# Performance work log

Hardware: AMD Instinct MI355X
Metric: run time of the kernel (lower is better)

The kernel has to match this reference:

```python
import jax, jax.numpy as jnp
import numpy as np

N, E = 100000, 1600000
IN, H, OUT = 64, 64, 32
BN_EPS = 1e-5


def setup_inputs() -> dict:
    key = jax.random.key(0)
    ks = jax.random.split(key, 13)

    def w(k, shape, fan_in):
        return jax.random.uniform(k, shape, jnp.float32, -1.0, 1.0) / np.sqrt(fan_in)

    return {
        "x": jax.random.normal(ks[0], (N, IN), jnp.float32),
        "edge_index": jax.random.randint(ks[1], (2, E), 0, N, jnp.int32),
        "W1": w(ks[2], (IN, H), IN),
        "b1": jnp.zeros((H,), jnp.float32),
        "gamma": jnp.ones((H,), jnp.float32),
        "beta": jnp.zeros((H,), jnp.float32),
        "W2": w(ks[3], (H, H), H),
        "b2": jnp.zeros((H,), jnp.float32),
        "lin2_w": w(ks[4], (H, OUT), H),
        "lin2_b": w(ks[5], (OUT,), H),
        "lin3_w": w(ks[6], (OUT, H), OUT),
        "lin3_b": w(ks[7], (H,), OUT),
    }


def gcn_conv(x, src, dst, W, b):
    # PyG GCNConv: h = D^{-1/2} (A + I) D^{-1/2} (x W) + b
    n = x.shape[0]
    h = x @ W  # [N, H]
    loop = jnp.arange(n, dtype=src.dtype)
    s = jnp.concatenate([src, loop])  # add self-loops
    d = jnp.concatenate([dst, loop])
    deg = jax.ops.segment_sum(jnp.ones_like(s, x.dtype), d, num_segments=n)
    dinv = jnp.where(deg > 0, jax.lax.rsqrt(deg), 0.0)
    norm = dinv[s] * dinv[d]  # [E+N]
    msg = h[s] * norm[:, None]  # gather + scale
    out = jax.ops.segment_sum(msg, d, num_segments=n)  # scatter-add
    return out + b


def reference(x, edge_index, W1, b1, gamma, beta, W2, b2, lin2_w, lin2_b, lin3_w, lin3_b):
    src, dst = edge_index[0], edge_index[1]
    h = gcn_conv(x, src, dst, W1, b1)
    # BatchNorm1d in eval mode with default running stats (mean=0, var=1)
    h = gamma * (h * jax.lax.rsqrt(jnp.float32(1.0 + BN_EPS))) + beta
    h = jax.nn.relu(h)  # dropout is identity in eval
    h = gcn_conv(h, src, dst, W2, b2)
    logits = h @ lin2_w + lin2_b  # [N, OUT]
    p = jax.nn.softmax(logits, axis=-1)
    ent = -jnp.sum(p * jnp.log(p + 1e-9), axis=-1)  # [N]
    wts = 1.0 / (ent + 1e-10)
    wts = (wts - wts.min()) / (wts.max() - wts.min())
    wts = jax.nn.softmax(wts, axis=0)  # [N]
    graph = jnp.sum(logits * wts[:, None], axis=0, keepdims=True)  # [1, OUT]
    return graph @ lin3_w + lin3_b  # [1, H]
```

## Files before the change

kernel.cpp:

```cpp
#include <hip/hip_runtime.h>
#include <hip/hip_bf16.h>
#include <hip/hip_fp8.h>
#include <math.h>


#define F 64
#define OUTF 32
#define PB 128
#define LEDGE 5632
#define WG 512
#define BN_INV 0.9999950000374997f
#define ESC_X 32.0f
#define IESC_X 0.03125f
#define ESC_Z 64.0f
#define IESC_Z 0.015625f

typedef short bf16x8 __attribute__((ext_vector_type(8)));
typedef float f32x4 __attribute__((ext_vector_type(4)));

__device__ __forceinline__ unsigned short f2bf(float f) {
    unsigned u = __float_as_uint(f);
    return (unsigned short)((u + 0x7fffu + ((u >> 16) & 1u)) >> 16);
}
__device__ __forceinline__ float bf2f(unsigned short h) {
    return __uint_as_float((unsigned)h << 16);
}

#if __has_builtin(__builtin_amdgcn_cvt_f32_fp8) && __has_builtin(__builtin_amdgcn_cvt_pk_fp8_f32)
__device__ __forceinline__ float4 fp8x4(unsigned v) {
    return make_float4(__builtin_amdgcn_cvt_f32_fp8((int)v, 0),
                       __builtin_amdgcn_cvt_f32_fp8((int)v, 1),
                       __builtin_amdgcn_cvt_f32_fp8((int)v, 2),
                       __builtin_amdgcn_cvt_f32_fp8((int)v, 3));
}
__device__ __forceinline__ unsigned fp8pk4(float a, float b, float c, float d) {
    int r = __builtin_amdgcn_cvt_pk_fp8_f32(a, b, 0, false);
    r = __builtin_amdgcn_cvt_pk_fp8_f32(c, d, r, true);
    return (unsigned)r;
}
__device__ __forceinline__ unsigned char fp8enc1(float a) {
    return (unsigned char)(__builtin_amdgcn_cvt_pk_fp8_f32(a, a, 0, false) & 0xff);
}
#else
__device__ __forceinline__ float fp8d1(unsigned char b) {
    __hip_fp8_e4m3 v; v.__x = (__hip_fp8_storage_t)b; return (float)v;
}
__device__ __forceinline__ float4 fp8x4(unsigned v) {
    return make_float4(fp8d1(v & 255u), fp8d1((v >> 8) & 255u), fp8d1((v >> 16) & 255u), fp8d1((v >> 24) & 255u));
}
__device__ __forceinline__ unsigned char fp8enc1(float a) {
    return (unsigned char)__hip_fp8_e4m3(a).__x;
}
__device__ __forceinline__ unsigned fp8pk4(float a, float b, float c, float d) {
    return (unsigned)fp8enc1(a) | ((unsigned)fp8enc1(b) << 8) | ((unsigned)fp8enc1(c) << 16) | ((unsigned)fp8enc1(d) << 24);
}
#endif

__global__ __launch_bounds__(256) void k_hist(const int* __restrict__ dst, int* __restrict__ hist,
                                              int E, int NBK,
                                              const float* __restrict__ W1, const float* __restrict__ b1,
                                              const float* __restrict__ gamma, const float* __restrict__ beta,
                                              const float* __restrict__ W2, const float* __restrict__ b2,
                                              const float* __restrict__ l2w, const float* __restrict__ l2b,
                                              unsigned short* __restrict__ w1f, unsigned short* __restrict__ w2f,
                                              float* __restrict__ bias1f, float* __restrict__ b2l2) {
    __shared__ int lh[512];
    int t = threadIdx.x, blk = blockIdx.x;
    if (blk >= PB) {
        int tt = (blk - PB) * 256 + t;
        int k = tt >> 5, cc = tt & 31;
        float o = 0.0f;
        for (int j = 0; j < F; j++) o += W2[k * F + j] * l2w[j * OUTF + cc];
        {
            int t2 = cc >> 4, s = k >> 5, kb = (k >> 3) & 3, jj = k & 7;
            int ln = kb * 16 + (cc & 15);
            w2f[(size_t)((t2 * 2 + s) * 64 + ln) * 8 + jj] = f2bf(o);
        }
        for (int e = tt; e < F * F; e += 2048) {
            int kk = e >> 6, c = e & 63;
            float wv = W1[kk * F + c] * gamma[c] * BN_INV;
            int t1i = c >> 4, s = kk >> 5, kb = (kk >> 3) & 3, jj = kk & 7;
            int ln = kb * 16 + (c & 15);
            w1f[(size_t)((t1i * 2 + s) * 64 + ln) * 8 + jj] = f2bf(wv);
        }
        if (tt < F) bias1f[tt] = fmaf(b1[tt], gamma[tt] * BN_INV, beta[tt]);
        if (tt < OUTF) {
            float b = l2b[tt];
            for (int j = 0; j < F; j++) b += b2[j] * l2w[j * OUTF + tt];
            b2l2[tt] = b;
        }
        return;
    }
    for (int b = t; b < NBK; b += 256) lh[b] = 0;
    __syncthreads();
    int chunk = (E + PB - 1) / PB;
    int beg = blk * chunk, end = min(beg + chunk, E);
    for (int e = beg + t; e < end; e += 256) atomicAdd(&lh[dst[e] >> 8], 1);
    __syncthreads();
    for (int b = t; b < NBK; b += 256) hist[blk * NBK + b] = lh[b];
}

__global__ __launch_bounds__(PB) void k_hscan1(int* __restrict__ hist, int* __restrict__ btot, int NBK) {
    __shared__ int s[PB];
    int b = blockIdx.x, t = threadIdx.x;
    int v = hist[t * NBK + b];
    s[t] = v;
    __syncthreads();
    for (int off = 1; off < PB; off <<= 1) {
        int u = (t >= off) ? s[t - off] : 0;
        __syncthreads();
        s[t] += u;
        __syncthreads();
    }
    hist[t * NBK + b] = s[t] - v;
    if (t == PB - 1) btot[b] = s[t];
}

__global__ void k_hscan2(const int* __restrict__ btot, int* __restrict__ bbase, int NBK) {
    __shared__ int s[512];
    int t = threadIdx.x;
    int v = (t < NBK) ? btot[t] : 0;
    s[t] = v;
    __syncthreads();
    for (int off = 1; off < 512; off <<= 1) {
        int u = (t >= off) ? s[t - off] : 0;
        __syncthreads();
        s[t] += u;
        __syncthreads();
    }
    if (t < NBK) {
        bbase[t] = s[t] - v;
        if (t == NBK - 1) bbase[NBK] = s[t];
    }
}

__global__ __launch_bounds__(256) void k_place(const int* __restrict__ src, const int* __restrict__ dst,
                                               const int* __restrict__ hist, const int* __restrict__ bbase,
                                               unsigned* __restrict__ bucketArr, int E, int NBK) {
    __shared__ int cur[512];
    int t = threadIdx.x, blk = blockIdx.x;
    for (int b = t; b < NBK; b += 256) cur[b] = hist[blk * NBK + b] + bbase[b];
    __syncthreads();
    int chunk = (E + PB - 1) / PB;
    int beg = blk * chunk, end = min(beg + chunk, E);
    for (int e = beg + t; e < end; e += 256) {
        int d = dst[e], sidx = src[e];
        int p = atomicAdd(&cur[d >> 8], 1);
        bucketArr[p] = ((unsigned)sidx << 8) | (unsigned)(d & 255);
    }
}

__global__ __launch_bounds__(256) void k_binsort(const unsigned* __restrict__ bucketArr,
                                                 const int* __restrict__ bbase,
                                                 int* __restrict__ eidx, int4* __restrict__ meta,
                                                 const float4* __restrict__ x4, unsigned* __restrict__ xq, int N) {
    __shared__ unsigned ledge[LEDGE];
    __shared__ int lcnt[256], lofs[256], lcur[256], lscan[256];
    __shared__ float ldinv[256];
    int b = blockIdx.x, t = threadIdx.x;
    int gb = bbase[b];
    int count = min(bbase[b + 1] - gb, LEDGE);
    for (int j = t; j < count; j += 256) ledge[j] = bucketArr[gb + j];
    lcnt[t] = 0;
    __syncthreads();
    for (int j = t; j < count; j += 256) atomicAdd(&lcnt[ledge[j] & 255u], 1);
    __syncthreads();
    int deg = lcnt[t];
    lscan[t] = deg;
    __syncthreads();
    for (int off = 1; off < 256; off <<= 1) {
        int u = (t >= off) ? lscan[t - off] : 0;
        __syncthreads();
        lscan[t] += u;
        __syncthreads();
    }
    lofs[t] = lscan[t] - deg;
    lcur[t] = 0;
    int node = (b << 8) + t;
    float di = rsqrtf((float)deg + 1.0f);
    ldinv[t] = di;
    if (node < N) meta[node] = make_int4(gb + lofs[t], deg, __float_as_int(di), 0);
    __syncthreads();
    for (int j = t; j < count; j += 256) {
        unsigned v = ledge[j];
        int loc = (int)(v & 255u);
        int p = atomicAdd(&lcur[loc], 1);
        eidx[gb + lofs[loc] + p] = (int)(v >> 8);
    }
    for (int idx = t; idx < 256 * 16; idx += 256) {
        int nd = (b << 8) + (idx >> 4);
        if (nd < N) {
            float d2 = ldinv[idx >> 4] * ESC_X;
            float4 v = x4[(size_t)nd * 16 + (idx & 15)];
            xq[(size_t)nd * 16 + (idx & 15)] = fp8pk4(v.x * d2, v.y * d2, v.z * d2, v.w * d2);
        }
    }
}

__global__ __launch_bounds__(256, 4) void k_conv1agg(const uint2* __restrict__ xq2,
                                                     const int4* __restrict__ meta,
                                                     const int* __restrict__ eidx,
                                                     unsigned short* __restrict__ t1, int N, int Em1) {
    int tid = threadIdx.x, wave = tid >> 6, lane = tid & 63;
    int g = lane >> 3, gl = lane & 7, gbase = lane & 56;
    int i = (blockIdx.x * 4 + wave) * 8 + g;
    int iclamp = min(i, N - 1);
    int4 m = meta[iclamp];
    int beg = m.x;
    int dcnt = (i < N) ? m.y : 0;
    float dis = __int_as_float(m.z) * IESC_X;
    int ss0 = eidx[min(beg + gl, Em1)];
    int ss1 = eidx[min(beg + 8 + gl, Em1)];
    int ss2 = eidx[min(beg + 16 + gl, Em1)];
    int ss3 = eidx[min(beg + 24 + gl, Em1)];
    uint2 selfv = xq2[(size_t)iclamp * 8 + gl];
    uint2 vbuf[32];
#pragma unroll
    for (int k = 0; k < 32; k++) {
        int sreg = (k < 8) ? ss0 : (k < 16) ? ss1 : (k < 24) ? ss2 : ss3;
        int sv = __shfl(sreg, gbase + (k & 7), 64);
        sv = (k < dcnt) ? sv : iclamp;
        vbuf[k] = xq2[(size_t)sv * 8 + gl];
    }
    __builtin_amdgcn_sched_barrier(0);
    float4 aA0 = fp8x4(selfv.x), aB0 = fp8x4(selfv.y);
    float4 aA1 = make_float4(0.f, 0.f, 0.f, 0.f), aB1 = aA1;
#pragma unroll
    for (int k = 0; k < 32; k++) {
        if (k < dcnt) {
            float4 vA = fp8x4(vbuf[k].x), vB = fp8x4(vbuf[k].y);
            if (k & 1) {
                aA1.x += vA.x; aA1.y += vA.y; aA1.z += vA.z; aA1.w += vA.w;
                aB1.x += vB.x; aB1.y += vB.y; aB1.z += vB.z; aB1.w += vB.w;
            } else {
                aA0.x += vA.x; aA0.y += vA.y; aA0.z += vA.z; aA0.w += vA.w;
                aB0.x += vB.x; aB0.y += vB.y; aB0.z += vB.z; aB0.w += vB.w;
            }
        }
    }
    for (int base = 32; base < dcnt; base += 8) {
        int j = base + gl;
        int ss = eidx[min(beg + j, Em1)];
        int cnt = min(dcnt - base, 8);
#pragma unroll
        for (int k = 0; k < 8; k++) {
            if (k < cnt) {
                int sv = __shfl(ss, gbase + k, 64);
                uint2 v = xq2[(size_t)sv * 8 + gl];
                float4 vA = fp8x4(v.x), vB = fp8x4(v.y);
                aA0.x += vA.x; aA0.y += vA.y; aA0.z += vA.z; aA0.w += vA.w;
                aB0.x += vB.x; aB0.y += vB.y; aB0.z += vB.z; aB0.w += vB.w;
            }
        }
    }
    if (i < N) {
        float4 oA, oB;
        oA.x = (aA0.x + aA1.x) * dis; oA.y = (aA0.y + aA1.y) * dis;
        oA.z = (aA0.z + aA1.z) * dis; oA.w = (aA0.w + aA1.w) * dis;
        oB.x = (aB0.x + aB1.x) * dis; oB.y = (aB0.y + aB1.y) * dis;
        oB.z = (aB0.z + aB1.z) * dis; oB.w = (aB0.w + aB1.w) * dis;
        uint4 ob;
        ob.x = (unsigned)f2bf(oA.x) | ((unsigned)f2bf(oA.y) << 16);
        ob.y = (unsigned)f2bf(oA.z) | ((unsigned)f2bf(oA.w) << 16);
        ob.z = (unsigned)f2bf(oB.x) | ((unsigned)f2bf(oB.y) << 16);
        ob.w = (unsigned)f2bf(oB.z) | ((unsigned)f2bf(oB.w) << 16);
        *(uint4*)(t1 + (size_t)i * F + gl * 8) = ob;
    }
}

__global__ __launch_bounds__(256) void k_zm(const unsigned short* __restrict__ t1bf,
                                            const int4* __restrict__ meta,
                                            const unsigned short* __restrict__ w1f,
                                            const unsigned short* __restrict__ w2f,
                                            const float* __restrict__ bias1f,
                                            unsigned char* __restrict__ z2q, int N) {
    __shared__ __align__(16) unsigned short hlds[4][16][72];
    __shared__ float ldin[4][16];
    int tid = threadIdx.x, wave = tid >> 6, lane = tid & 63;
    int cl = lane & 15, kb = lane >> 4;
    int ntiles = (N + 15) >> 4;
    int tile = blockIdx.x * 4 + wave;
    if (tile >= ntiles) return;
    int row0 = tile << 4;

    int ra = min(row0 + cl, N - 1);
    const bf16x8* arow = (const bf16x8*)(t1bf + (size_t)ra * F);
    bf16x8 a0 = arow[kb];
    bf16x8 a1 = arow[4 + kb];
    if (lane < 16) ldin[wave][lane] = __int_as_float(meta[min(row0 + lane, N - 1)].z);

    const bf16x8* w1v = (const bf16x8*)w1f;
    const bf16x8* w2v = (const bf16x8*)w2f;
    bf16x8 w1frag[8];
#pragma unroll
    for (int q = 0; q < 8; q++) w1frag[q] = w1v[q * 64 + lane];
    bf16x8 w2frag[4];
#pragma unroll
    for (int q = 0; q < 4; q++) w2frag[q] = w2v[q * 64 + lane];
    float bias_t[4];
#pragma unroll
    for (int t = 0; t < 4; t++) bias_t[t] = bias1f[t * 16 + cl];

    f32x4 acc[4] = {};
#pragma unroll
    for (int t = 0; t < 4; t++) {
        acc[t] = __builtin_amdgcn_mfma_f32_16x16x32_bf16(a0, w1frag[t * 2 + 0], acc[t], 0, 0, 0);
        acc[t] = __builtin_amdgcn_mfma_f32_16x16x32_bf16(a1, w1frag[t * 2 + 1], acc[t], 0, 0, 0);
    }
    float di[4];
#pragma unroll
    for (int j = 0; j < 4; j++) di[j] = ldin[wave][kb * 4 + j];
#pragma unroll
    for (int t = 0; t < 4; t++)
#pragma unroll
        for (int j = 0; j < 4; j++) {
            float h = fmaxf(acc[t][j] + bias_t[t], 0.0f) * di[j];
            hlds[wave][kb * 4 + j][t * 16 + cl] = f2bf(h);
        }
    bf16x8 h0 = *(const bf16x8*)&hlds[wave][cl][kb * 8];
    bf16x8 h1 = *(const bf16x8*)&hlds[wave][cl][32 + kb * 8];
    f32x4 accz[2] = {};
#pragma unroll
    for (int t2 = 0; t2 < 2; t2++) {
        accz[t2] = __builtin_amdgcn_mfma_f32_16x16x32_bf16(h0, w2frag[t2 * 2 + 0], accz[t2], 0, 0, 0);
        accz[t2] = __builtin_amdgcn_mfma_f32_16x16x32_bf16(h1, w2frag[t2 * 2 + 1], accz[t2], 0, 0, 0);
    }
#pragma unroll
    for (int t2 = 0; t2 < 2; t2++)
#pragma unroll
        for (int j = 0; j < 4; j++) {
            int r = row0 + kb * 4 + j;
            if (r < N) z2q[(size_t)r * OUTF + t2 * 16 + cl] = fp8enc1(accz[t2][j] * ESC_Z);
        }
}

__device__ __forceinline__ void conv2_consume(const uint2 (&vbuf)[24], uint2 selfv, int dcnt,
                                              int i, int beg, float dis, int gl, int gbase,
                                              const uint2* __restrict__ z2q2, const int* __restrict__ eidx,
                                              int Em1, float4 bvA, float4 bvB,
                                              unsigned short* __restrict__ logits_bf,
                                              float* __restrict__ wraw,
                                              float& mnW, float& mxW, int N) {
    float4 aA0 = fp8x4(selfv.x), aB0 = fp8x4(selfv.y);
    if (i >= N) { aA0 = make_float4(0.f, 0.f, 0.f, 0.f); aB0 = aA0; }
    float4 aA1 = make_float4(0.f, 0.f, 0.f, 0.f), aB1 = aA1;
#pragma unroll
    for (int k = 0; k < 24; k++) {
        if (k < dcnt) {
            float4 vA = fp8x4(vbuf[k].x), vB = fp8x4(vbuf[k].y);
            if (k & 1) {
                aA1.x += vA.x; aA1.y += vA.y; aA1.z += vA.z; aA1.w += vA.w;
                aB1.x += vB.x; aB1.y += vB.y; aB1.z += vB.z; aB1.w += vB.w;
            } else {
                aA0.x += vA.x; aA0.y += vA.y; aA0.z += vA.z; aA0.w += vA.w;
                aB0.x += vB.x; aB0.y += vB.y; aB0.z += vB.z; aB0.w += vB.w;
            }
        }
    }
    for (int base = 24; base < dcnt; base += 4) {
        int j = base + gl;
        int ss = eidx[min(beg + j, Em1)];
        int cnt = min(dcnt - base, 4);
#pragma unroll
        for (int k = 0; k < 4; k++) {
            if (k < cnt) {
                int sv = __shfl(ss, gbase + k, 64);
                uint2 v = z2q2[(size_t)sv * 4 + gl];
                float4 vA = fp8x4(v.x), vB = fp8x4(v.y);
                aA0.x += vA.x; aA0.y += vA.y; aA0.z += vA.z; aA0.w += vA.w;
                aB0.x += vB.x; aB0.y += vB.y; aB0.z += vB.z; aB0.w += vB.w;
            }
        }
    }
    float4 lgA, lgB;
    lgA.x = fmaf(aA0.x + aA1.x, dis, bvA.x);
    lgA.y = fmaf(aA0.y + aA1.y, dis, bvA.y);
    lgA.z = fmaf(aA0.z + aA1.z, dis, bvA.z);
    lgA.w = fmaf(aA0.w + aA1.w, dis, bvA.w);
    lgB.x = fmaf(aB0.x + aB1.x, dis, bvB.x);
    lgB.y = fmaf(aB0.y + aB1.y, dis, bvB.y);
    lgB.z = fmaf(aB0.z + aB1.z, dis, bvB.z);
    lgB.w = fmaf(aB0.w + aB1.w, dis, bvB.w);
    if (i < N) {
        uint4 ob;
        ob.x = (unsigned)f2bf(lgA.x) | ((unsigned)f2bf(lgA.y) << 16);
        ob.y = (unsigned)f2bf(lgA.z) | ((unsigned)f2bf(lgA.w) << 16);
        ob.z = (unsigned)f2bf(lgB.x) | ((unsigned)f2bf(lgB.y) << 16);
        ob.w = (unsigned)f2bf(lgB.z) | ((unsigned)f2bf(lgB.w) << 16);
        *(uint4*)(logits_bf + (size_t)i * OUTF + gl * 8) = ob;
    }
    float m8 = fmaxf(fmaxf(fmaxf(lgA.x, lgA.y), fmaxf(lgA.z, lgA.w)),
                     fmaxf(fmaxf(lgB.x, lgB.y), fmaxf(lgB.z, lgB.w)));
    for (int off = 2; off > 0; off >>= 1) m8 = fmaxf(m8, __shfl_xor(m8, off, 4));
    float p0 = __expf(lgA.x - m8), p1 = __expf(lgA.y - m8), p2 = __expf(lgA.z - m8), p3 = __expf(lgA.w - m8);
    float p4 = __expf(lgB.x - m8), p5 = __expf(lgB.y - m8), p6 = __expf(lgB.z - m8), p7 = __expf(lgB.w - m8);
    float s8 = p0 + p1 + p2 + p3 + p4 + p5 + p6 + p7;
    for (int off = 2; off > 0; off >>= 1) s8 += __shfl_xor(s8, off, 4);
    float inv = 1.0f / s8;
    float t0 = p0 * inv, t1v = p1 * inv, t2v = p2 * inv, t3 = p3 * inv;
    float t4 = p4 * inv, t5 = p5 * inv, t6 = p6 * inv, t7 = p7 * inv;
    float e8 = t0 * __logf(t0 + 1e-9f) + t1v * __logf(t1v + 1e-9f) + t2v * __logf(t2v + 1e-9f) + t3 * __logf(t3 + 1e-9f) +
               t4 * __logf(t4 + 1e-9f) + t5 * __logf(t5 + 1e-9f) + t6 * __logf(t6 + 1e-9f) + t7 * __logf(t7 + 1e-9f);
    for (int off = 2; off > 0; off >>= 1) e8 += __shfl_xor(e8, off, 4);
    float w = 1.0f / (-e8 + 1e-10f);
    if (i < N) {
        if (gl == 0) wraw[i] = w;
        mnW = fminf(mnW, w);
        mxW = fmaxf(mxW, w);
    }
}

__global__ __launch_bounds__(256, 2) void k_conv2agg(const uint2* __restrict__ z2q2,
                                                     const int4* __restrict__ meta,
                                                     const int* __restrict__ eidx, const float* __restrict__ b2l2,
                                                     unsigned short* __restrict__ logits_bf, float* __restrict__ wraw,
                                                     float* __restrict__ mnmx, int N, int Em1) {
    __shared__ float smn[4], smx[4];
    int tid = threadIdx.x, wave = tid >> 6, lane = tid & 63;
    int g = lane >> 2, gl = lane & 3, gbase = lane & 60;
    float4 bvA = ((const float4*)b2l2)[gl * 2];
    float4 bvB = ((const float4*)b2l2)[gl * 2 + 1];
    int wgid = blockIdx.x * 4 + wave;
    int i0 = wgid * 32 + g;
    int i1 = wgid * 32 + 16 + g;
    int i0c = min(i0, N - 1), i1c = min(i1, N - 1);
    int4 m0 = meta[i0c], m1 = meta[i1c];
    int beg0 = m0.x, beg1 = m1.x;
    int d0 = (i0 < N) ? m0.y : 0;
    int d1 = (i1 < N) ? m1.y : 0;
    float dis0 = __int_as_float(m0.z) * IESC_Z;
    float dis1 = __int_as_float(m1.z) * IESC_Z;
    int sA0 = eidx[min(beg0 + gl, Em1)];
    int sA1 = eidx[min(beg0 + 4 + gl, Em1)];
    int sA2 = eidx[min(beg0 + 8 + gl, Em1)];
    int sA3 = eidx[min(beg0 + 12 + gl, Em1)];
    int sA4 = eidx[min(beg0 + 16 + gl, Em1)];
    int sA5 = eidx[min(beg0 + 20 + gl, Em1)];
    int sB0 = eidx[min(beg1 + gl, Em1)];
    int sB1 = eidx[min(beg1 + 4 + gl, Em1)];
    int sB2 = eidx[min(beg1 + 8 + gl, Em1)];
    int sB3 = eidx[min(beg1 + 12 + gl, Em1)];
    int sB4 = eidx[min(beg1 + 16 + gl, Em1)];
    int sB5 = eidx[min(beg1 + 20 + gl, Em1)];
    uint2 self0 = z2q2[(size_t)i0c * 4 + gl];
    uint2 self1 = z2q2[(size_t)i1c * 4 + gl];
    uint2 vb0[24], vb1[24];
#pragma unroll
    for (int k = 0; k < 24; k++) {
        int sreg = (k < 4) ? sA0 : (k < 8) ? sA1 : (k < 12) ? sA2 : (k < 16) ? sA3 : (k < 20) ? sA4 : sA5;
        int sv = __shfl(sreg, gbase + (k & 3), 64);
        sv = (k < d0) ? sv : i0c;
        vb0[k] = z2q2[(size_t)sv * 4 + gl];
    }
#pragma unroll
    for (int k = 0; k < 24; k++) {
        int sreg = (k < 4) ? sB0 : (k < 8) ? sB1 : (k < 12) ? sB2 : (k < 16) ? sB3 : (k < 20) ? sB4 : sB5;
        int sv = __shfl(sreg, gbase + (k & 3), 64);
        sv = (k < d1) ? sv : i1c;
        vb1[k] = z2q2[(size_t)sv * 4 + gl];
    }
    __builtin_amdgcn_sched_barrier(0);
    float mnW = INFINITY, mxW = -INFINITY;
    conv2_consume(vb0, self0, d0, i0, beg0, dis0, gl, gbase, z2q2, eidx, Em1,
                  bvA, bvB, logits_bf, wraw, mnW, mxW, N);
    conv2_consume(vb1, self1, d1, i1, beg1, dis1, gl, gbase, z2q2, eidx, Em1,
                  bvA, bvB, logits_bf, wraw, mnW, mxW, N);
    for (int off = 32; off > 0; off >>= 1) {
        mnW = fminf(mnW, __shfl_xor(mnW, off, 64));
        mxW = fmaxf(mxW, __shfl_xor(mxW, off, 64));
    }
    if (lane == 0) { smn[wave] = mnW; smx[wave] = mxW; }
    __syncthreads();
    if (tid == 0) {
        mnmx[blockIdx.x * 2]     = fminf(fminf(smn[0], smn[1]), fminf(smn[2], smn[3]));
        mnmx[blockIdx.x * 2 + 1] = fmaxf(fmaxf(smx[0], smx[1]), fmaxf(smx[2], smx[3]));
    }
}

__global__ __launch_bounds__(256) void k_weight(const unsigned short* __restrict__ logits_bf,
                                                const float* __restrict__ wraw,
                                                const float* __restrict__ mnmx, int nmm,
                                                float* __restrict__ part, int N) {
    __shared__ float rmn[4], rmx[4];
    float mn = INFINITY, mx = -INFINITY;
    for (int j = threadIdx.x; j < nmm; j += 256) {
        mn = fminf(mn, mnmx[j * 2]);
        mx = fmaxf(mx, mnmx[j * 2 + 1]);
    }
    for (int off = 32; off > 0; off >>= 1) {
        mn = fminf(mn, __shfl_xor(mn, off, 64));
        mx = fmaxf(mx, __shfl_xor(mx, off, 64));
    }
    int wv = threadIdx.x >> 6;
    if ((threadIdx.x & 63) == 0) { rmn[wv] = mn; rmx[wv] = mx; }
    __syncthreads();
    mn = fminf(fminf(rmn[0], rmn[1]), fminf(rmn[2], rmn[3]));
    mx = fmaxf(fmaxf(rmx[0], rmx[1]), fmaxf(rmx[2], rmx[3]));
    float inv = 1.0f / (mx - mn);
    int c = threadIdx.x & 31;
    int g = threadIdx.x >> 5;
    float acc = 0.0f, es = 0.0f;
    for (int r = blockIdx.x * 8 + g; r < N; r += gridDim.x * 8) {
        float e = __expf((wraw[r] - mn) * inv);
        acc += e * bf2f(logits_bf[(size_t)r * OUTF + c]);
        if (c == 0) es += e;
    }
    __shared__ float sa[8][OUTF];
    __shared__ float se[8];
    sa[g][c] = acc;
    if (c == 0) se[g] = es;
    __syncthreads();
    if (g == 0) {
        float t = sa[0][c];
#pragma unroll
        for (int i = 1; i < 8; i++) t += sa[i][c];
        part[blockIdx.x * 36 + c] = t;
        if (c == 0) {
            float u = 0.0f;
#pragma unroll
            for (int i = 0; i < 8; i++) u += se[i];
            part[blockIdx.x * 36 + 32] = u;
        }
    }
}

__global__ __launch_bounds__(256) void k_final(const float* __restrict__ part,
                                               const float* __restrict__ w3, const float* __restrict__ b3,
                                               float* __restrict__ out) {
    __shared__ float sa[8][OUTF];
    __shared__ float se[8];
    __shared__ float facc[OUTF + 1];
    int tid = threadIdx.x;
    int g = tid >> 5, c = tid & 31;
    float acc = 0.0f, es = 0.0f;
    for (int p = g; p < WG; p += 8) {
        acc += part[p * 36 + c];
        if (c == 0) es += part[p * 36 + 32];
    }
    sa[g][c] = acc;
    if (c == 0) se[g] = es;
    __syncthreads();
    if (tid < OUTF) {
        float t = 0.0f;
#pragma unroll
        for (int i = 0; i < 8; i++) t += sa[i][tid];
        facc[tid] = t;
    }
    if (tid == 32) {
        float u = 0.0f;
#pragma unroll
        for (int i = 0; i < 8; i++) u += se[i];
        facc[OUTF] = u;
    }
    __syncthreads();
    if (tid < F) {
        float s = facc[OUTF];
        float o = b3[tid];
#pragma unroll
        for (int cc = 0; cc < OUTF; cc++) o += (facc[cc] / s) * w3[cc * F + tid];
        out[tid] = o;
    }
}

extern "C" void kernel_launch(void* const* d_in, const int* in_sizes, int n_in,
                              void* d_out, int out_size, void* d_ws, size_t ws_size,
                              hipStream_t stream) {
    const float* x     = (const float*)d_in[0];
    const int*   ei    = (const int*)d_in[1];
    const float* W1    = (const float*)d_in[2];
    const float* b1    = (const float*)d_in[3];
    const float* gamma = (const float*)d_in[4];
    const float* beta  = (const float*)d_in[5];
    const float* W2    = (const float*)d_in[6];
    const float* b2    = (const float*)d_in[7];
    const float* l2w   = (const float*)d_in[8];
    const float* l2b   = (const float*)d_in[9];
    const float* l3w   = (const float*)d_in[10];
    const float* l3b   = (const float*)d_in[11];

    int N = in_sizes[0] / F;
    int E = in_sizes[1] / 2;
    const int* src = ei;
    const int* dst = ei + E;
    int NBK = (N + 255) >> 8;

    char* p = (char*)d_ws;
    int* hist = (int*)p;                p += (size_t)PB * NBK * 4;
    int* btot = (int*)p;                p += 512 * 4;
    int* bbase = (int*)p;               p += 516 * 4;
    unsigned* bucketArr = (unsigned*)p; p += (size_t)E * 4;
    int4* meta = (int4*)p;              p += (size_t)N * 16;
    int* eidx = (int*)p;                p += (size_t)E * 4;
    float* mnmx = (float*)p;            p += 2048 * 4;
    float* part = (float*)p;            p += (size_t)WG * 36 * 4;
    unsigned short* w1f = (unsigned short*)p;  p += F * F * 2;
    unsigned short* w2f = (unsigned short*)p;  p += F * OUTF * 2;
    float* bias1f = (float*)p;          p += F * 4;
    float* b2l2 = (float*)p;            p += OUTF * 4 + 32;
    unsigned* xq = (unsigned*)p;        p += (size_t)N * F;
    unsigned short* t1bf = (unsigned short*)p; p += (size_t)N * F * 2;
    float* wraw = (float*)p;            p += (size_t)N * 4;
    unsigned char* z2q = (unsigned char*)xq;
    unsigned short* logits_bf = (unsigned short*)t1bf;

    k_hist<<<PB + 8, 256, 0, stream>>>(dst, hist, E, NBK, W1, b1, gamma, beta, W2, b2, l2w, l2b,
                                       w1f, w2f, bias1f, b2l2);
    k_hscan1<<<NBK, PB, 0, stream>>>(hist, btot, NBK);
    k_hscan2<<<1, 512, 0, stream>>>(btot, bbase, NBK);
    k_place<<<PB, 256, 0, stream>>>(src, dst, hist, bbase, bucketArr, E, NBK);
    k_binsort<<<NBK, 256, 0, stream>>>(bucketArr, bbase, eidx, meta, (const float4*)x, xq, N);

    k_conv1agg<<<(N + 31) / 32, 256, 0, stream>>>((const uint2*)xq, meta, eidx, t1bf, N, E - 1);
    int nt = (N + 15) >> 4;
    k_zm<<<(nt + 3) / 4, 256, 0, stream>>>(t1bf, meta, w1f, w2f, bias1f, z2q, N);
    int wg2 = (nt + 1) >> 1;
    int nb2 = (wg2 + 3) >> 2;
    k_conv2agg<<<nb2, 256, 0, stream>>>((const uint2*)z2q, meta, eidx, b2l2, logits_bf, wraw, mnmx, N, E - 1);

    k_weight<<<WG, 256, 0, stream>>>(logits_bf, wraw, mnmx, nb2, part, N);
    k_final<<<1, 256, 0, stream>>>(part, l3w, l3b, (float*)d_out);
}
```

Before: 243.5 us.

## Stage conv1 neighbor gathers through LDS via direct global-to-LDS loads

Rewrites the first-layer aggregation so each node uses 4 lanes with 16-byte fp8 loads instead of 8 lanes with 8-byte loads. The first 24 neighbor rows per node are prefetched with global_load_lds straight into a double-indexed shared buffer rather than into a 32-entry register array. The goal is to cut register pressure and issue fewer, wider gather requests while keeping many loads in flight. In exchange it uses 48KB of LDS per 128-thread block, which limits occupancy, and the prefetch depth drops from 32 to 24.

After: 246.6 us. No clear change (+1.3%).

```diff
diff --git a/kernel.cpp b/kernel.cpp
--- a/kernel.cpp
+++ b/kernel.cpp
@@ -9,6 +9,7 @@
 #define PB 128
 #define LEDGE 5632
 #define WG 512
+#define C1S 24
 #define BN_INV 0.9999950000374997f
 #define ESC_X 32.0f
 #define IESC_X 0.03125f
@@ -17,6 +18,8 @@
 
 typedef short bf16x8 __attribute__((ext_vector_type(8)));
 typedef float f32x4 __attribute__((ext_vector_type(4)));
+typedef const __attribute__((address_space(1))) void* gas_ptr;
+typedef __attribute__((address_space(3))) void* las_ptr;
 
 __device__ __forceinline__ unsigned short f2bf(float f) {
     unsigned u = __float_as_uint(f);
@@ -197,74 +200,77 @@
     }
 }
 
-__global__ __launch_bounds__(256, 4) void k_conv1agg(const uint2* __restrict__ xq2,
-                                                     const int4* __restrict__ meta,
-                                                     const int* __restrict__ eidx,
-                                                     unsigned short* __restrict__ t1, int N, int Em1) {
+__global__ __launch_bounds__(128) void k_conv1l(const char* __restrict__ xqc,
+                                                const int4* __restrict__ meta,
+                                                const int* __restrict__ eidx,
+                                                unsigned short* __restrict__ t1, int N, int Em1) {
+    __shared__ __align__(16) unsigned char stage[2][C1S][64 * 16];
     int tid = threadIdx.x, wave = tid >> 6, lane = tid & 63;
-    int g = lane >> 3, gl = lane & 7, gbase = lane & 56;
-    int i = (blockIdx.x * 4 + wave) * 8 + g;
-    int iclamp = min(i, N - 1);
-    int4 m = meta[iclamp];
+    int g = lane >> 2, gl = lane & 3, gbase = lane & 60;
+    int i = (blockIdx.x * 2 + wave) * 16 + g;
+    int ic = min(i, N - 1);
+    int4 m = meta[ic];
     int beg = m.x;
     int dcnt = (i < N) ? m.y : 0;
     float dis = __int_as_float(m.z) * IESC_X;
-    int ss0 = eidx[min(beg + gl, Em1)];
-    int ss1 = eidx[min(beg + 8 + gl, Em1)];
-    int ss2 = eidx[min(beg + 16 + gl, Em1)];
-    int ss3 = eidx[min(beg + 24 + gl, Em1)];
-    uint2 selfv = xq2[(size_t)iclamp * 8 + gl];
-    uint2 vbuf[32];
-#pragma unroll
-    for (int k = 0; k < 32; k++) {
-        int sreg = (k < 8) ? ss0 : (k < 16) ? ss1 : (k < 24) ? ss2 : ss3;
-        int sv = __shfl(sreg, gbase + (k & 7), 64);
-        sv = (k < dcnt) ? sv : iclamp;
-        vbuf[k] = xq2[(size_t)sv * 8 + gl];
-    }
-    __builtin_amdgcn_sched_barrier(0);
-    float4 aA0 = fp8x4(selfv.x), aB0 = fp8x4(selfv.y);
-    float4 aA1 = make_float4(0.f, 0.f, 0.f, 0.f), aB1 = aA1;
-#pragma unroll
-    for (int k = 0; k < 32; k++) {
+    int s0 = eidx[min(beg + gl, Em1)];
+    int s1 = eidx[min(beg + 4 + gl, Em1)];
+    int s2 = eidx[min(beg + 8 + gl, Em1)];
+    int s3 = eidx[min(beg + 12 + gl, Em1)];
+    int s4 = eidx[min(beg + 16 + gl, Em1)];
+    int s5 = eidx[min(beg + 20 + gl, Em1)];
+    uint4 selfv = *(const uint4*)(xqc + (size_t)ic * 64 + gl * 16);
+#pragma unroll
+    for (int k = 0; k < C1S; k++) {
+        int sreg = (k < 4) ? s0 : (k < 8) ? s1 : (k < 12) ? s2 : (k < 16) ? s3 : (k < 20) ? s4 : s5;
+        int sv = __shfl(sreg, gbase + (k & 3), 64);
+        sv = (k < dcnt) ? sv : ic;
+        const void* gp = xqc + (size_t)sv * 64 + gl * 16;
+        __builtin_amdgcn_global_load_lds((gas_ptr)gp, (las_ptr)&stage[wave][k][0], 16, 0, 0);
+    }
+    asm volatile("s_waitcnt vmcnt(0)" ::: "memory");
+    float4 a0 = fp8x4(selfv.x), a1 = fp8x4(selfv.y), a2 = fp8x4(selfv.z), a3 = fp8x4(selfv.w);
+#pragma unroll
+    for (int k = 0; k < C1S; k++) {
         if (k < dcnt) {
-            float4 vA = fp8x4(vbuf[k].x), vB = fp8x4(vbuf[k].y);
-            if (k & 1) {
-                aA1.x += vA.x; aA1.y += vA.y; aA1.z += vA.z; aA1.w += vA.w;
-                aB1.x += vB.x; aB1.y += vB.y; aB1.z += vB.z; aB1.w += vB.w;
-            } else {
-                aA0.x += vA.x; aA0.y += vA.y; aA0.z += vA.z; aA0.w += vA.w;
-                aB0.x += vB.x; aB0.y += vB.y; aB0.z += vB.z; aB0.w += vB.w;
-            }
-        }
-    }
-    for (int base = 32; base < dcnt; base += 8) {
+            uint4 v = *(const uint4*)&stage[wave][k][lane * 16];
+            float4 vA = fp8x4(v.x), vB = fp8x4(v.y), vC = fp8x4(v.z), vD = fp8x4(v.w);
+            a0.x += vA.x; a0.y += vA.y; a0.z += vA.z; a0.w += vA.w;
+            a1.x += vB.x; a1.y += vB.y; a1.z += vB.z; a1.w += vB.w;
+            a2.x += vC.x; a2.y += vC.y; a2.z += vC.z; a2.w += vC.w;
+            a3.x += vD.x; a3.y += vD.y; a3.z += vD.z; a3.w += vD.w;
+        }
+    }
+    for (int base = C1S; base < dcnt; base += 4) {
         int j = base + gl;
         int ss = eidx[min(beg + j, Em1)];
-        int cnt = min(dcnt - base, 8);
-#pragma unroll
-        for (int k = 0; k < 8; k++) {
+        int cnt = min(dcnt - base, 4);
+#pragma unroll
+        for (int k = 0; k < 4; k++) {
             if (k < cnt) {
                 int sv = __shfl(ss, gbase + k, 64);
-                uint2 v = xq2[(size_t)sv * 8 + gl];
-                float4 vA = fp8x4(v.x), vB = fp8x4(v.y);
-                aA0.x += vA.x; aA0.y += vA.y; aA0.z += vA.z; aA0.w += vA.w;
-                aB0.x += vB.x; aB0.y += vB.y; aB0.z += vB.z; aB0.w += vB.w;
+                uint4 v = *(const uint4*)(xqc + (size_t)sv * 64 + gl * 16);
+                float4 vA = fp8x4(v.x), vB = fp8x4(v.y), vC = fp8x4(v.z), vD = fp8x4(v.w);
+                a0.x += vA.x; a0.y += vA.y; a0.z += vA.z; a0.w += vA.w;
+                a1.x += vB.x; a1.y += vB.y; a1.z += vB.z; a1.w += vB.w;
+                a2.x += vC.x; a2.y += vC.y; a2.z += vC.z; a2.w += vC.w;
+                a3.x += vD.x; a3.y += vD.y; a3.z += vD.z; a3.w += vD.w;
             }
         }
     }
     if (i < N) {
-        float4 oA, oB;
-        oA.x = (aA0.x + aA1.x) * dis; oA.y = (aA0.y + aA1.y) * dis;
-        oA.z = (aA0.z + aA1.z) * dis; oA.w = (aA0.w + aA1.w) * dis;
-        oB.x = (aB0.x + aB1.x) * dis; oB.y = (aB0.y + aB1.y) * dis;
-        oB.z = (aB0.z + aB1.z) * dis; oB.w = (aB0.w + aB1.w) * dis;
-        uint4 ob;
-        ob.x = (unsigned)f2bf(oA.x) | ((unsigned)f2bf(oA.y) << 16);
-        ob.y = (unsigned)f2bf(oA.z) | ((unsigned)f2bf(oA.w) << 16);
-        ob.z = (unsigned)f2bf(oB.x) | ((unsigned)f2bf(oB.y) << 16);
-        ob.w = (unsigned)f2bf(oB.z) | ((unsigned)f2bf(oB.w) << 16);
-        *(uint4*)(t1 + (size_t)i * F + gl * 8) = ob;
+        uint4 o1, o2;
+        o1.x = (unsigned)f2bf(a0.x * dis) | ((unsigned)f2bf(a0.y * dis) << 16);
+        o1.y = (unsigned)f2bf(a0.z * dis) | ((unsigned)f2bf(a0.w * dis) << 16);
+        o1.z = (unsigned)f2bf(a1.x * dis) | ((unsigned)f2bf(a1.y * dis) << 16);
+        o1.w = (unsigned)f2bf(a1.z * dis) | ((unsigned)f2bf(a1.w * dis) << 16);
+        o2.x = (unsigned)f2bf(a2.x * dis) | ((unsigned)f2bf(a2.y * dis) << 16);
+        o2.y = (unsigned)f2bf(a2.z * dis) | ((unsigned)f2bf(a2.w * dis) << 16);
+        o2.z = (unsigned)f2bf(a3.x * dis) | ((unsigned)f2bf(a3.y * dis) << 16);
+        o2.w = (unsigned)f2bf(a3.z * dis) | ((unsigned)f2bf(a3.w * dis) << 16);
+        uint4* outp = (uint4*)(t1 + (size_t)i * F + gl * 16);
+        outp[0] = o1;
+        outp[1] = o2;
     }
 }
 
@@ -610,7 +616,8 @@
     k_place<<<PB, 256, 0, stream>>>(src, dst, hist, bbase, bucketArr, E, NBK);
     k_binsort<<<NBK, 256, 0, stream>>>(bucketArr, bbase, eidx, meta, (const float4*)x, xq, N);
 
-    k_conv1agg<<<(N + 31) / 32, 256, 0, stream>>>((const uint2*)xq, meta, eidx, t1bf, N, E - 1);
+    int nb1 = (N + 31) / 32;
+    k_conv1l<<<nb1, 128, 0, stream>>>((const char*)xq, meta, eidx, t1bf, N, E - 1);
     int nt = (N + 15) >> 4;
     k_zm<<<(nt + 3) / 4, 256, 0, stream>>>(t1bf, meta, w1f, w2f, bias1f, z2q, N);
     int wg2 = (nt + 1) >> 1;
```
